# Kernel optimization log

Hardware: AMD Instinct MI355X
Metric: run time of the kernel (lower is better)

Reference implementation:

```python
import jax, jax.numpy as jnp
import numpy as np

N = 16384
IN_F = 256
OUT_F = 128
ALPHA = 0.2  # leaky relu negative slope
NEG = -9e15


def _xavier(key, shape, gain=1.414):
    fan_in, fan_out = shape
    a = gain * np.sqrt(6.0 / (fan_in + fan_out))
    return jax.random.uniform(key, shape, jnp.float32, -a, a)


def setup_inputs() -> dict:
    key = jax.random.key(0)
    k_h, k_adj, k_q, k_k, k_v = jax.random.split(key, 5)
    h = jax.random.normal(k_h, (N, IN_F), dtype=jnp.float32)
    adj = jax.random.randint(k_adj, (N, N), 0, 2, dtype=jnp.int32)
    W_query = _xavier(k_q, (IN_F, OUT_F))
    W_key = _xavier(k_k, (IN_F, OUT_F))
    W_value = _xavier(k_v, (IN_F, OUT_F))
    return {"h": h, "adj": adj, "W_query": W_query, "W_key": W_key, "W_value": W_value}


def reference(h, adj, W_query, W_key, W_value):
    # h: [N, in], adj: [N, N] 0/1
    Q = h @ W_query           # [N, out]
    K = h @ W_key             # [N, out]
    V = h @ W_value           # [N, out]
    e = jnp.einsum('nd,md->nm', Q, K)          # [N, N]
    e = jnp.where(e >= 0, e, ALPHA * e)         # leaky relu
    e = jnp.where(adj > 0, e, NEG)              # adjacency mask
    attention = jax.nn.softmax(e, axis=1)       # row softmax
    # dropout: eval mode (training=False) -> identity
    h_prime = attention @ V                     # [N, out]
    return jax.nn.elu(h_prime)                  # concat=True
```

## Files before the change

kernel.cpp:

```cpp
#include <hip/hip_runtime.h>

#define N_TOK 16384
#define ALPHA_LRELU 0.2f
#define NEGV -9e15f
#define NSPLIT 3
#define LOG2E 1.44269504f

typedef _Float16 f16;
typedef __attribute__((ext_vector_type(8))) _Float16 f16x8;
typedef __attribute__((ext_vector_type(4))) float f32x4;
typedef __attribute__((ext_vector_type(4))) int i32x4;
typedef unsigned short u16;

__device__ __forceinline__ float bf2f(u16 b) {
  unsigned u = ((unsigned)b) << 16;
  return __builtin_bit_cast(float, u);
}
__device__ __forceinline__ f16x8 cvt8(i32x4 v) {
  f16x8 r;
#pragma unroll
  for (int i = 0; i < 4; ++i) {
    unsigned u = __builtin_bit_cast(unsigned, v[i]);
    r[2 * i]     = (f16)__builtin_bit_cast(float, (u & 0xffffu) << 16);
    r[2 * i + 1] = (f16)__builtin_bit_cast(float, u & 0xffff0000u);
  }
  return r;
}

__global__ __launch_bounds__(64) void detect_kernel(const u16* __restrict__ h16,
                                                    int* __restrict__ flag)
{
  int lane = threadIdx.x;
  unsigned u = h16[lane * 2];
  unsigned e = (u >> 7) & 0xFFu;
  int sane = (e >= 0x60u && e <= 0x8Eu) ? 1 : 0;
#pragma unroll
  for (int off = 32; off >= 1; off >>= 1) sane += __shfl_xor(sane, off);
  if (lane == 0) *flag = (sane >= 32) ? 1 : 0;
}

__global__ __launch_bounds__(256) void sentinel_kernel(float* __restrict__ out) {
  int i = blockIdx.x * 256 + threadIdx.x;
  if (i < N_TOK * 128) out[i] = 100.0f;
}

__global__ __launch_bounds__(256) void wt_kernel(
    const int* __restrict__ flag,
    const void* __restrict__ Wq, const void* __restrict__ Wk,
    const void* __restrict__ Wv, f16* __restrict__ Wt)
{
  const int isbf = *flag;
  int w = blockIdx.y;
  const void* W = (w == 0) ? Wq : (w == 1) ? Wk : Wv;
  int idx = blockIdx.x * 256 + threadIdx.x;
  int k = idx >> 7, n = idx & 127;
  float v = isbf ? bf2f(((const u16*)W)[idx]) : ((const float*)W)[idx];
  if (w == 0) v *= LOG2E;
  Wt[w * 32768 + n * 256 + k] = (f16)v;
}

__global__ __launch_bounds__(256) void qkv_kernel(
    const int* __restrict__ flag, const void* __restrict__ hvp,
    const f16* __restrict__ Wt,
    f16* __restrict__ Qo, f16* __restrict__ Ko, f16* __restrict__ Vt)
{
  const int isbf = *flag;
  const int mb = blockIdx.x * 64;
  const int gy = blockIdx.y;
  const int tid = threadIdx.x;
  const int wave = tid >> 6, lane = tid & 63, quad = lane >> 4, l16 = lane & 15;

  __shared__ __align__(16) f16 hs[64][256 + 8];

  if (isbf) {
    const u16* h = (const u16*)hvp;
#pragma unroll
    for (int i = 0; i < 8; ++i) {
      int c = i * 256 + tid;
      int r = c >> 5, o = c & 31;
      i32x4 v = *(const i32x4*)(h + (size_t)(mb + r) * 256 + o * 8);
      *(f16x8*)(&hs[r][o * 8]) = cvt8(v);
    }
  } else {
    const float* h = (const float*)hvp;
#pragma unroll
    for (int i = 0; i < 8; ++i) {
      int c = i * 256 + tid;
      int r = c >> 5, o = c & 31;
      const float* p = h + (size_t)(mb + r) * 256 + o * 8;
      f32x4 v0 = *(const f32x4*)p, v1 = *(const f32x4*)(p + 4);
      f16x8 q;
#pragma unroll
      for (int j = 0; j < 4; ++j) { q[j] = (f16)v0[j]; q[4 + j] = (f16)v1[j]; }
      *(f16x8*)(&hs[r][o * 8]) = q;
    }
  }
  __syncthreads();

  const f16* Wg = Wt + gy * 32768;

  if (gy < 2) {
    f16x8 a[8];
#pragma unroll
    for (int ks = 0; ks < 8; ++ks)
      a[ks] = *(const f16x8*)(&hs[wave * 16 + l16][ks * 32 + quad * 8]);
    f32x4 acc[8];
#pragma unroll
    for (int ct = 0; ct < 8; ++ct) acc[ct] = (f32x4){0.f, 0.f, 0.f, 0.f};
#pragma unroll
    for (int ks = 0; ks < 8; ++ks)
#pragma unroll
      for (int ct = 0; ct < 8; ++ct) {
        f16x8 b = *(const f16x8*)(Wg + (ct * 16 + l16) * 256 + ks * 32 + quad * 8);
        acc[ct] = __builtin_amdgcn_mfma_f32_16x16x32_f16(a[ks], b, acc[ct], 0, 0, 0);
      }
    f16* O = (gy == 0) ? Qo : Ko;
#pragma unroll
    for (int ct = 0; ct < 8; ++ct)
#pragma unroll
      for (int r = 0; r < 4; ++r)
        O[(size_t)(mb + wave * 16 + quad * 4 + r) * 128 + ct * 16 + l16] = (f16)acc[ct][r];
  } else {
    f32x4 acc[2][4];
#pragma unroll
    for (int ft = 0; ft < 2; ++ft)
#pragma unroll
      for (int bt = 0; bt < 4; ++bt) acc[ft][bt] = (f32x4){0.f, 0.f, 0.f, 0.f};
#pragma unroll
    for (int ks = 0; ks < 8; ++ks) {
      f16x8 a2[2], b2[4];
#pragma unroll
      for (int ft = 0; ft < 2; ++ft)
        a2[ft] = *(const f16x8*)(Wg + ((wave * 2 + ft) * 16 + l16) * 256 + ks * 32 + quad * 8);
#pragma unroll
      for (int bt = 0; bt < 4; ++bt)
        b2[bt] = *(const f16x8*)(&hs[bt * 16 + l16][ks * 32 + quad * 8]);
#pragma unroll
      for (int ft = 0; ft < 2; ++ft)
#pragma unroll
        for (int bt = 0; bt < 4; ++bt)
          acc[ft][bt] = __builtin_amdgcn_mfma_f32_16x16x32_f16(a2[ft], b2[bt], acc[ft][bt], 0, 0, 0);
    }
#pragma unroll
    for (int ft = 0; ft < 2; ++ft)
#pragma unroll
      for (int bt = 0; bt < 4; ++bt)
#pragma unroll
        for (int r = 0; r < 4; ++r)
          Vt[(size_t)((wave * 2 + ft) * 16 + quad * 4 + r) * N_TOK + mb + bt * 16 + l16] =
              (f16)acc[ft][bt][r];
  }
}

__global__ __launch_bounds__(256, 2) void flash_kernel(
    const f16* __restrict__ Q, const f16* __restrict__ Kg,
    const f16* __restrict__ Vt, const int* __restrict__ adj,
    float* __restrict__ Opart, float* __restrict__ mpart,
    float* __restrict__ lpart)
{
  const int qb = blockIdx.x * 64;
  const int ksec = blockIdx.y;
  const int base = 256 / NSPLIT;
  const int rem  = 256 % NSPLIT;
  const int iters = base + (ksec < rem ? 1 : 0);
  const int tile0 = ksec * base + (ksec < rem ? ksec : rem);
  const int kb0 = tile0 * 64;
  const int tid = threadIdx.x;
  const int wave = tid >> 6, lane = tid & 63, quad = lane >> 4, l16 = lane & 15;

  __shared__ __align__(16) f16 Ks[64][136];
  __shared__ __align__(16) f16 Vs[128][72];
  __shared__ __align__(16) f16 Ps[4][16][72];
  __shared__ __align__(8)  u16 As16[64][4];

  f16x8 qf[4];
#pragma unroll
  for (int ks = 0; ks < 4; ++ks)
    qf[ks] = *(const f16x8*)(Q + (size_t)(qb + wave * 16 + l16) * 128 + ks * 32 + quad * 8);

  f16x8 ONES;
#pragma unroll
  for (int j = 0; j < 8; ++j) ONES[j] = (f16)1.0f;

  const int shq = (l16 & 3) * 16 + (l16 >> 2);

  f32x4 Oacc[8];
#pragma unroll
  for (int ot = 0; ot < 8; ++ot) Oacc[ot] = (f32x4){0.f, 0.f, 0.f, 0.f};
  f32x4 Lacc = (f32x4){0.f, 0.f, 0.f, 0.f};
  float m2[4];
#pragma unroll
  for (int r = 0; r < 4; ++r) m2[r] = -INFINITY;

  i32x4 pK[4], pV[4], pA[4];
#pragma unroll
  for (int i = 0; i < 4; ++i) {
    int c = i * 256 + tid;
    pK[i] = *(const i32x4*)(Kg + (size_t)(kb0 + (c >> 4)) * 128 + (c & 15) * 8);
    pV[i] = *(const i32x4*)(Vt + (size_t)(c >> 3) * N_TOK + kb0 + (c & 7) * 8);
    pA[i] = *(const i32x4*)(adj + (size_t)(qb + (c >> 4)) * N_TOK + kb0 + (c & 15) * 4);
  }

  for (int it = 0; it < iters; ++it) {
    __syncthreads();
#pragma unroll
    for (int i = 0; i < 4; ++i) {
      int c = i * 256 + tid;
      *(f16x8*)(&Ks[c >> 4][(c & 15) * 8]) = __builtin_bit_cast(f16x8, pK[i]);
      *(f16x8*)(&Vs[c >> 3][(c & 7) * 8])  = __builtin_bit_cast(f16x8, pV[i]);
      unsigned long long b0 = __ballot(pA[i][0] > 0);
      unsigned long long b1 = __ballot(pA[i][1] > 0);
      unsigned long long b2 = __ballot(pA[i][2] > 0);
      unsigned long long b3 = __ballot(pA[i][3] > 0);
      if (lane < 16) {
        int j = lane & 3, g = lane >> 2;
        unsigned long long v = (j == 0) ? b0 : (j == 1) ? b1 : (j == 2) ? b2 : b3;
        As16[i * 16 + wave * 4 + g][j] = (u16)(v >> (16 * g));
      }
    }
    __syncthreads();
    if (it + 1 < iters) {
      int kb = kb0 + (it + 1) * 64;
#pragma unroll
      for (int i = 0; i < 4; ++i) {
        int c = i * 256 + tid;
        pK[i] = *(const i32x4*)(Kg + (size_t)(kb + (c >> 4)) * 128 + (c & 15) * 8);
        pV[i] = *(const i32x4*)(Vt + (size_t)(c >> 3) * N_TOK + kb + (c & 7) * 8);
        pA[i] = *(const i32x4*)(adj + (size_t)(qb + (c >> 4)) * N_TOK + kb + (c & 15) * 4);
      }
    }

    float sc[4][4];
#pragma unroll
    for (int ct = 0; ct < 4; ++ct) {
      f32x4 s = (f32x4){0.f, 0.f, 0.f, 0.f};
#pragma unroll
      for (int ks = 0; ks < 4; ++ks) {
        f16x8 b = *(const f16x8*)(&Ks[ct * 16 + l16][ks * 32 + quad * 8]);
        s = __builtin_amdgcn_mfma_f32_16x16x32_f16(qf[ks], b, s, 0, 0, 0);
      }
#pragma unroll
      for (int r = 0; r < 4; ++r) {
        float v = s[r];
        sc[ct][r] = fmaxf(v, ALPHA_LRELU * v);
      }
    }
#pragma unroll
    for (int r = 0; r < 4; ++r) {
      unsigned long long a64 =
          *(const unsigned long long*)(&As16[wave * 16 + quad * 4 + r][0]);
      unsigned y = (unsigned)(a64 >> shq);
#pragma unroll
      for (int ct = 0; ct < 4; ++ct)
        if (!((y >> (4 * ct)) & 1u)) sc[ct][r] = NEGV;
    }

    float mx[4];
#pragma unroll
    for (int r = 0; r < 4; ++r) {
      float m = fmaxf(fmaxf(sc[0][r], sc[1][r]), fmaxf(sc[2][r], sc[3][r]));
#pragma unroll
      for (int off = 8; off >= 1; off >>= 1)
        m = fmaxf(m, __shfl_xor(m, off, 16));
      mx[r] = m;
    }
    bool up = (mx[0] > m2[0]) | (mx[1] > m2[1]) | (mx[2] > m2[2]) | (mx[3] > m2[3]);
    if (__ballot(up)) {
      float al[4];
#pragma unroll
      for (int r = 0; r < 4; ++r) {
        float mn = fmaxf(m2[r], mx[r]);
        al[r] = exp2f(m2[r] - mn);
        m2[r] = mn;
      }
#pragma unroll
      for (int ot = 0; ot < 8; ++ot)
#pragma unroll
        for (int r = 0; r < 4; ++r) Oacc[ot][r] *= al[r];
#pragma unroll
      for (int r = 0; r < 4; ++r) Lacc[r] *= al[r];
    }

#pragma unroll
    for (int ct = 0; ct < 4; ++ct)
#pragma unroll
      for (int r = 0; r < 4; ++r)
        Ps[wave][quad * 4 + r][ct * 16 + l16] = (f16)exp2f(sc[ct][r] - m2[r]);

    asm volatile("s_waitcnt lgkmcnt(0)" ::: "memory");
    f16x8 pa0 = *(const f16x8*)(&Ps[wave][l16][quad * 8]);
    f16x8 pa1 = *(const f16x8*)(&Ps[wave][l16][32 + quad * 8]);
#pragma unroll
    for (int ot = 0; ot < 8; ++ot) {
      f16x8 b0 = *(const f16x8*)(&Vs[ot * 16 + l16][quad * 8]);
      f16x8 b1 = *(const f16x8*)(&Vs[ot * 16 + l16][32 + quad * 8]);
      Oacc[ot] = __builtin_amdgcn_mfma_f32_16x16x32_f16(pa0, b0, Oacc[ot], 0, 0, 0);
      Oacc[ot] = __builtin_amdgcn_mfma_f32_16x16x32_f16(pa1, b1, Oacc[ot], 0, 0, 0);
    }
    Lacc = __builtin_amdgcn_mfma_f32_16x16x32_f16(pa0, ONES, Lacc, 0, 0, 0);
    Lacc = __builtin_amdgcn_mfma_f32_16x16x32_f16(pa1, ONES, Lacc, 0, 0, 0);
  }

  float* Op = Opart + (size_t)ksec * (N_TOK * 128);
#pragma unroll
  for (int ot = 0; ot < 8; ++ot)
#pragma unroll
    for (int r = 0; r < 4; ++r) {
      int row = qb + wave * 16 + quad * 4 + r;
      Op[(size_t)row * 128 + ot * 16 + l16] = Oacc[ot][r];
    }
  if (l16 == 0) {
#pragma unroll
    for (int r = 0; r < 4; ++r) {
      int row = qb + wave * 16 + quad * 4 + r;
      mpart[ksec * N_TOK + row] = m2[r];
      lpart[ksec * N_TOK + row] = Lacc[r];
    }
  }
}

__global__ __launch_bounds__(256) void combine_kernel(
    const float* __restrict__ Opart, const float* __restrict__ mpart,
    const float* __restrict__ lpart, float* __restrict__ out)
{
  const int qb = blockIdx.x * 64;
  const int t = threadIdx.x;
  __shared__ float sa[NSPLIT][64], sdn[64];
  if (t < 64) {
    float m = -INFINITY;
#pragma unroll
    for (int s = 0; s < NSPLIT; ++s) m = fmaxf(m, mpart[s * N_TOK + qb + t]);
    float dn = 0.f;
#pragma unroll
    for (int s = 0; s < NSPLIT; ++s) {
      float a = exp2f(mpart[s * N_TOK + qb + t] - m);
      sa[s][t] = a;
      dn += lpart[s * N_TOK + qb + t] * a;
    }
    sdn[t] = 1.0f / dn;
  }
  __syncthreads();
  float* Og = out + (size_t)qb * 128;
#pragma unroll
  for (int i = 0; i < 8; ++i) {
    int idx = (i * 256 + t) * 4;
    int row = idx >> 7;
    f32x4 acc = (f32x4){0.f, 0.f, 0.f, 0.f};
#pragma unroll
    for (int s = 0; s < NSPLIT; ++s) {
      f32x4 o = *(const f32x4*)(Opart + (size_t)s * (N_TOK * 128) + (size_t)qb * 128 + idx);
      float a = sa[s][row];
#pragma unroll
      for (int j = 0; j < 4; ++j) acc[j] += o[j] * a;
    }
    float dn = sdn[row];
    f32x4 v;
#pragma unroll
    for (int j = 0; j < 4; ++j) {
      float x = acc[j] * dn;
      v[j] = (x > 0.f) ? x : (__expf(x) - 1.f);
    }
    *(f32x4*)(Og + idx) = v;
  }
}

__global__ __launch_bounds__(256) void flash1_kernel(
    const f16* __restrict__ Q, const f16* __restrict__ Kg,
    const f16* __restrict__ Vt, const int* __restrict__ adj,
    float* __restrict__ out)
{
  const int qb = blockIdx.x * 64;
  const int tid = threadIdx.x;
  const int wave = tid >> 6, lane = tid & 63, quad = lane >> 4, l16 = lane & 15;

  __shared__ __align__(16) f16 Ks[64][136];
  __shared__ __align__(16) f16 Vs[128][72];
  __shared__ __align__(16) int As[64][68];
  __shared__ __align__(16) f16 Ps[4][16][72];

  f16x8 qf[4];
#pragma unroll
  for (int ks = 0; ks < 4; ++ks)
    qf[ks] = *(const f16x8*)(Q + (size_t)(qb + wave * 16 + l16) * 128 + ks * 32 + quad * 8);
  f16x8 ONES;
#pragma unroll
  for (int j = 0; j < 8; ++j) ONES[j] = (f16)1.0f;

  f32x4 Oacc[8];
#pragma unroll
  for (int ot = 0; ot < 8; ++ot) Oacc[ot] = (f32x4){0.f, 0.f, 0.f, 0.f};
  f32x4 Lacc = (f32x4){0.f, 0.f, 0.f, 0.f};
  float m2[4];
#pragma unroll
  for (int r = 0; r < 4; ++r) m2[r] = -INFINITY;

  i32x4 pK[4], pV[4], pA[4];
#pragma unroll
  for (int i = 0; i < 4; ++i) {
    int c = i * 256 + tid;
    pK[i] = *(const i32x4*)(Kg + (size_t)(c >> 4) * 128 + (c & 15) * 8);
    pV[i] = *(const i32x4*)(Vt + (size_t)(c >> 3) * N_TOK + (c & 7) * 8);
    pA[i] = *(const i32x4*)(adj + (size_t)(qb + (c >> 4)) * N_TOK + (c & 15) * 4);
  }

  for (int it = 0; it < 256; ++it) {
    __syncthreads();
#pragma unroll
    for (int i = 0; i < 4; ++i) {
      int c = i * 256 + tid;
      *(f16x8*)(&Ks[c >> 4][(c & 15) * 8]) = __builtin_bit_cast(f16x8, pK[i]);
      *(f16x8*)(&Vs[c >> 3][(c & 7) * 8])  = __builtin_bit_cast(f16x8, pV[i]);
      *(i32x4*)(&As[c >> 4][(c & 15) * 4]) = pA[i];
    }
    __syncthreads();
    if (it + 1 < 256) {
      int kb = (it + 1) * 64;
#pragma unroll
      for (int i = 0; i < 4; ++i) {
        int c = i * 256 + tid;
        pK[i] = *(const i32x4*)(Kg + (size_t)(kb + (c >> 4)) * 128 + (c & 15) * 8);
        pV[i] = *(const i32x4*)(Vt + (size_t)(c >> 3) * N_TOK + kb + (c & 7) * 8);
        pA[i] = *(const i32x4*)(adj + (size_t)(qb + (c >> 4)) * N_TOK + kb + (c & 15) * 4);
      }
    }
    float sc[4][4];
#pragma unroll
    for (int ct = 0; ct < 4; ++ct) {
      f32x4 s = (f32x4){0.f, 0.f, 0.f, 0.f};
#pragma unroll
      for (int ks = 0; ks < 4; ++ks) {
        f16x8 b = *(const f16x8*)(&Ks[ct * 16 + l16][ks * 32 + quad * 8]);
        s = __builtin_amdgcn_mfma_f32_16x16x32_f16(qf[ks], b, s, 0, 0, 0);
      }
#pragma unroll
      for (int r = 0; r < 4; ++r) {
        float v = s[r];
        v = fmaxf(v, ALPHA_LRELU * v);
        sc[ct][r] = (As[wave * 16 + quad * 4 + r][ct * 16 + l16] > 0) ? v : NEGV;
      }
    }
    float mx[4];
#pragma unroll
    for (int r = 0; r < 4; ++r) {
      float m = fmaxf(fmaxf(sc[0][r], sc[1][r]), fmaxf(sc[2][r], sc[3][r]));
#pragma unroll
      for (int off = 8; off >= 1; off >>= 1)
        m = fmaxf(m, __shfl_xor(m, off, 16));
      mx[r] = m;
    }
    bool up = (mx[0] > m2[0]) | (mx[1] > m2[1]) | (mx[2] > m2[2]) | (mx[3] > m2[3]);
    if (__ballot(up)) {
      float al[4];
#pragma unroll
      for (int r = 0; r < 4; ++r) {
        float mn = fmaxf(m2[r], mx[r]);
        al[r] = exp2f(m2[r] - mn);
        m2[r] = mn;
      }
#pragma unroll
      for (int ot = 0; ot < 8; ++ot)
#pragma unroll
        for (int r = 0; r < 4; ++r) Oacc[ot][r] *= al[r];
#pragma unroll
      for (int r = 0; r < 4; ++r) Lacc[r] *= al[r];
    }
#pragma unroll
    for (int ct = 0; ct < 4; ++ct)
#pragma unroll
      for (int r = 0; r < 4; ++r)
        Ps[wave][quad * 4 + r][ct * 16 + l16] = (f16)exp2f(sc[ct][r] - m2[r]);

    asm volatile("s_waitcnt lgkmcnt(0)" ::: "memory");
    f16x8 pa0 = *(const f16x8*)(&Ps[wave][l16][quad * 8]);
    f16x8 pa1 = *(const f16x8*)(&Ps[wave][l16][32 + quad * 8]);
#pragma unroll
    for (int ot = 0; ot < 8; ++ot) {
      f16x8 b0 = *(const f16x8*)(&Vs[ot * 16 + l16][quad * 8]);
      f16x8 b1 = *(const f16x8*)(&Vs[ot * 16 + l16][32 + quad * 8]);
      Oacc[ot] = __builtin_amdgcn_mfma_f32_16x16x32_f16(pa0, b0, Oacc[ot], 0, 0, 0);
      Oacc[ot] = __builtin_amdgcn_mfma_f32_16x16x32_f16(pa1, b1, Oacc[ot], 0, 0, 0);
    }
    Lacc = __builtin_amdgcn_mfma_f32_16x16x32_f16(pa0, ONES, Lacc, 0, 0, 0);
    Lacc = __builtin_amdgcn_mfma_f32_16x16x32_f16(pa1, ONES, Lacc, 0, 0, 0);
  }
#pragma unroll
  for (int ot = 0; ot < 8; ++ot)
#pragma unroll
    for (int r = 0; r < 4; ++r) {
      float v = Oacc[ot][r] / Lacc[r];
      v = (v > 0.f) ? v : (__expf(v) - 1.f);
      int row = qb + wave * 16 + quad * 4 + r;
      out[(size_t)row * 128 + ot * 16 + l16] = v;
    }
}

extern "C" void kernel_launch(void* const* d_in, const int* in_sizes, int n_in,
                              void* d_out, int out_size, void* d_ws, size_t ws_size,
                              hipStream_t stream)
{
  const void* h  = d_in[0];
  const int* adj = (const int*)d_in[1];
  const void* Wq = d_in[2];
  const void* Wk = d_in[3];
  const void* Wv = d_in[4];
  float* out = (float*)d_out;

  char* ws = (char*)d_ws;
  int* flag = (int*)ws;
  f16* Wt = (f16*)(ws + 1024);
  f16* Q  = (f16*)(ws + 262144);
  f16* K  = (f16*)(ws + 4456448);
  f16* Vt = (f16*)(ws + 8650752);
  float* Opart = (float*)(ws + 12845056);
  float* mpart = (float*)(ws + 38010880);
  float* lpart = (float*)(ws + 38207488);
  const size_t NEED_BASE  = 12845056;
  const size_t NEED_SPLIT = 38404096;

  if (ws_size < NEED_BASE) {
    sentinel_kernel<<<(N_TOK * 128 + 255) / 256, 256, 0, stream>>>(out);
    return;
  }

  detect_kernel<<<1, 64, 0, stream>>>((const u16*)h, flag);
  wt_kernel<<<dim3(128, 3), 256, 0, stream>>>(flag, Wq, Wk, Wv, Wt);
  qkv_kernel<<<dim3(256, 3), 256, 0, stream>>>(flag, h, Wt, Q, K, Vt);

  if (ws_size >= NEED_SPLIT) {
    flash_kernel<<<dim3(256, NSPLIT), 256, 0, stream>>>(Q, K, Vt, adj,
                                                        Opart, mpart, lpart);
    combine_kernel<<<dim3(256), 256, 0, stream>>>(Opart, mpart, lpart, out);
  } else {
    flash1_kernel<<<dim3(256), 256, 0, stream>>>(Q, K, Vt, adj, out);
  }
}
```

Before: 1.598 ms.

## Prepack adjacency into bitmasks in a separate kernel before flash attention

Adds a prepack kernel that reads the int32 adjacency matrix once and writes a bit-packed u64 mask per row and 64-key tile, laid out so each lane can test its own bits directly. The flash kernel then loads packed masks instead of streaming int32 adjacency through registers, ballots and shared memory, which removes in-loop ballot work and an LDS buffer. The split factor drops from three to two because the flash kernel now carries less memory traffic. The cost is an extra kernel launch and about 32 MB of workspace, and the flash path now runs only when the workspace is larger.

```diff
diff --git a/kernel.cpp b/kernel.cpp
--- a/kernel.cpp
+++ b/kernel.cpp
@@ -3,7 +3,7 @@
 #define N_TOK 16384
 #define ALPHA_LRELU 0.2f
 #define NEGV -9e15f
-#define NSPLIT 3
+#define NSPLIT 2
 #define LOG2E 1.44269504f
 
 typedef _Float16 f16;
@@ -11,6 +11,7 @@
 typedef __attribute__((ext_vector_type(4))) float f32x4;
 typedef __attribute__((ext_vector_type(4))) int i32x4;
 typedef unsigned short u16;
+typedef unsigned long long u64;
 
 __device__ __forceinline__ float bf2f(u16 b) {
   unsigned u = ((unsigned)b) << 16;
@@ -59,6 +60,36 @@
   Wt[w * 32768 + n * 256 + k] = (f16)v;
 }
 
+__global__ __launch_bounds__(256) void prepack_kernel(
+    const int* __restrict__ adj, u64* __restrict__ adjp)
+{
+  const int lane = threadIdx.x & 63;
+  const int gwave = blockIdx.x * 4 + (threadIdx.x >> 6);
+  const int nwave = gridDim.x * 4;
+  const int total_macro = N_TOK * 64;
+  for (int m = gwave; m < total_macro; m += nwave) {
+    int r  = m >> 6;
+    int t4 = (m & 63) * 4;
+    const int* base = adj + (size_t)r * N_TOK + t4 * 64 + lane;
+    u64 b[4];
+#pragma unroll
+    for (int u = 0; u < 4; ++u) {
+      int v = base[u * 64];
+      b[u] = __ballot(v > 0);
+    }
+    if (lane == 0) {
+      u64* dst = adjp + (size_t)r * 256 + t4;
+      i32x4 w0, w1;
+      w0[0] = (int)(unsigned)b[0]; w0[1] = (int)(b[0] >> 32);
+      w0[2] = (int)(unsigned)b[1]; w0[3] = (int)(b[1] >> 32);
+      w1[0] = (int)(unsigned)b[2]; w1[1] = (int)(b[2] >> 32);
+      w1[2] = (int)(unsigned)b[3]; w1[3] = (int)(b[3] >> 32);
+      *(i32x4*)dst       = w0;
+      *(i32x4*)(dst + 2) = w1;
+    }
+  }
+}
+
 __global__ __launch_bounds__(256) void qkv_kernel(
     const int* __restrict__ flag, const void* __restrict__ hvp,
     const f16* __restrict__ Wt,
@@ -154,7 +185,7 @@
 
 __global__ __launch_bounds__(256, 2) void flash_kernel(
     const f16* __restrict__ Q, const f16* __restrict__ Kg,
-    const f16* __restrict__ Vt, const int* __restrict__ adj,
+    const f16* __restrict__ Vt, const u64* __restrict__ adjp,
     float* __restrict__ Opart, float* __restrict__ mpart,
     float* __restrict__ lpart)
 {
@@ -171,7 +202,6 @@
   __shared__ __align__(16) f16 Ks[64][136];
   __shared__ __align__(16) f16 Vs[128][72];
   __shared__ __align__(16) f16 Ps[4][16][72];
-  __shared__ __align__(8)  u16 As16[64][4];
 
   f16x8 qf[4];
 #pragma unroll
@@ -182,7 +212,7 @@
 #pragma unroll
   for (int j = 0; j < 8; ++j) ONES[j] = (f16)1.0f;
 
-  const int shq = (l16 & 3) * 16 + (l16 >> 2);
+  const u64* aprow = adjp + (size_t)(qb + wave * 16 + quad * 4) * 256 + tile0;
 
   f32x4 Oacc[8];
 #pragma unroll
@@ -192,13 +222,12 @@
 #pragma unroll
   for (int r = 0; r < 4; ++r) m2[r] = -INFINITY;
 
-  i32x4 pK[4], pV[4], pA[4];
+  i32x4 pK[4], pV[4];
 #pragma unroll
   for (int i = 0; i < 4; ++i) {
     int c = i * 256 + tid;
     pK[i] = *(const i32x4*)(Kg + (size_t)(kb0 + (c >> 4)) * 128 + (c & 15) * 8);
     pV[i] = *(const i32x4*)(Vt + (size_t)(c >> 3) * N_TOK + kb0 + (c & 7) * 8);
-    pA[i] = *(const i32x4*)(adj + (size_t)(qb + (c >> 4)) * N_TOK + kb0 + (c & 15) * 4);
   }
 
   for (int it = 0; it < iters; ++it) {
@@ -208,17 +237,11 @@
       int c = i * 256 + tid;
       *(f16x8*)(&Ks[c >> 4][(c & 15) * 8]) = __builtin_bit_cast(f16x8, pK[i]);
       *(f16x8*)(&Vs[c >> 3][(c & 7) * 8])  = __builtin_bit_cast(f16x8, pV[i]);
-      unsigned long long b0 = __ballot(pA[i][0] > 0);
-      unsigned long long b1 = __ballot(pA[i][1] > 0);
-      unsigned long long b2 = __ballot(pA[i][2] > 0);
-      unsigned long long b3 = __ballot(pA[i][3] > 0);
-      if (lane < 16) {
-        int j = lane & 3, g = lane >> 2;
-        unsigned long long v = (j == 0) ? b0 : (j == 1) ? b1 : (j == 2) ? b2 : b3;
-        As16[i * 16 + wave * 4 + g][j] = (u16)(v >> (16 * g));
-      }
     }
     __syncthreads();
+    u64 au[4];
+#pragma unroll
+    for (int r = 0; r < 4; ++r) au[r] = aprow[(size_t)r * 256 + it];
     if (it + 1 < iters) {
       int kb = kb0 + (it + 1) * 64;
 #pragma unroll
@@ -226,7 +249,6 @@
         int c = i * 256 + tid;
         pK[i] = *(const i32x4*)(Kg + (size_t)(kb + (c >> 4)) * 128 + (c & 15) * 8);
         pV[i] = *(const i32x4*)(Vt + (size_t)(c >> 3) * N_TOK + kb + (c & 7) * 8);
-        pA[i] = *(const i32x4*)(adj + (size_t)(qb + (c >> 4)) * N_TOK + kb + (c & 15) * 4);
       }
     }
 
@@ -247,12 +269,12 @@
     }
 #pragma unroll
     for (int r = 0; r < 4; ++r) {
-      unsigned long long a64 =
-          *(const unsigned long long*)(&As16[wave * 16 + quad * 4 + r][0]);
-      unsigned y = (unsigned)(a64 >> shq);
-#pragma unroll
-      for (int ct = 0; ct < 4; ++ct)
-        if (!((y >> (4 * ct)) & 1u)) sc[ct][r] = NEGV;
+      unsigned lo = (unsigned)au[r], hi = (unsigned)(au[r] >> 32);
+      unsigned ta = lo >> l16, tb = hi >> l16;
+      if (!(ta & 1u))       sc[0][r] = NEGV;
+      if (!(ta & 0x10000u)) sc[1][r] = NEGV;
+      if (!(tb & 1u))       sc[2][r] = NEGV;
+      if (!(tb & 0x10000u)) sc[3][r] = NEGV;
     }
 
     float mx[4];
@@ -511,11 +533,12 @@
   f16* Q  = (f16*)(ws + 262144);
   f16* K  = (f16*)(ws + 4456448);
   f16* Vt = (f16*)(ws + 8650752);
-  float* Opart = (float*)(ws + 12845056);
-  float* mpart = (float*)(ws + 38010880);
-  float* lpart = (float*)(ws + 38207488);
+  u64* adjp = (u64*)(ws + 12845056);
+  float* Opart = (float*)(ws + 46399488);
+  float* mpart = (float*)(ws + 63176704);
+  float* lpart = (float*)(ws + 63307776);
   const size_t NEED_BASE  = 12845056;
-  const size_t NEED_SPLIT = 38404096;
+  const size_t NEED_SPLIT = 63438848;
 
   if (ws_size < NEED_BASE) {
     sentinel_kernel<<<(N_TOK * 128 + 255) / 256, 256, 0, stream>>>(out);
@@ -527,7 +550,8 @@
   qkv_kernel<<<dim3(256, 3), 256, 0, stream>>>(flag, h, Wt, Q, K, Vt);
 
   if (ws_size >= NEED_SPLIT) {
-    flash_kernel<<<dim3(256, NSPLIT), 256, 0, stream>>>(Q, K, Vt, adj,
+    prepack_kernel<<<2048, 256, 0, stream>>>(adj, adjp);
+    flash_kernel<<<dim3(256, NSPLIT), 256, 0, stream>>>(Q, K, Vt, adjp,
                                                         Opart, mpart, lpart);
     combine_kernel<<<dim3(256), 256, 0, stream>>>(Opart, mpart, lpart, out);
   } else {
```

Result: slower. 1.773 ms (+10.9%).
